# Optimization experiments

Hardware: AMD Instinct MI355X
Metric: run time of the kernel (lower is better)

## Reference

```python
import jax, jax.numpy as jnp
import numpy as np

THETA = 1.2
XI = 0.3


def setup_inputs() -> dict:
    key = jax.random.key(0)
    k1, k2 = jax.random.split(key)
    B, D = 8192, 512
    x = jax.random.normal(k1, (B, D), dtype=jnp.float32)
    y = jax.random.randint(k2, (B,), 0, 1000, dtype=jnp.int64)
    return {"x": x, "y": y}


def reference(x, y):
    B = x.shape[0]
    # per-sample L2 normalization: n_i = x_i / ||x_i||
    n = x / jnp.linalg.norm(x, axis=1, keepdims=True)  # [B, D]
    # pairwise squared distances ||n_i - n_j||^2 = |n_i|^2 + |n_j|^2 - 2 n_i.n_j
    sq = jnp.sum(n * n, axis=1)                        # [B]
    G = n @ n.T                                        # [B, B]
    dist2 = sq[:, None] + sq[None, :] - 2.0 * G        # [B, B]
    # indicator: +1 if same label else -1 (symmetric)
    ind = jnp.where(y[:, None] == y[None, :], 1.0, -1.0)
    # original loops i in [0,B), j in [i,B): upper triangle including diagonal
    idx = jnp.arange(B)
    mask = (idx[None, :] >= idx[:, None]).astype(x.dtype)
    hinge = jnp.maximum(THETA - dist2, 0.0)
    total = jnp.sum(mask * (XI + ind * hinge))
    m_scalar = 1.0 / (B * B - B)
    return m_scalar * total
```

## Files before the change

kernel.cpp:

```cpp
#include <hip/hip_runtime.h>
#include <cstdint>
#include <cstddef>

#define THETA 1.2f
#define XI 0.3f
#define BDIM 8192
#define DDIM 512
#define NWORK 544
#define NPAIRS_UP (((double)BDIM * (double)(BDIM + 1)) * 0.5)

typedef float f32x4 __attribute__((ext_vector_type(4)));
typedef int i32x8 __attribute__((ext_vector_type(8)));

__global__ __launch_bounds__(256) void normalize_rows(
    const float* __restrict__ x, unsigned char* __restrict__ nf8,
    float* __restrict__ sq, unsigned int* __restrict__ counter)
{
    if (blockIdx.x == 0 && threadIdx.x == 0) { *counter = 0u; }
    int row = blockIdx.x * 4 + (threadIdx.x >> 6);
    int l = threadIdx.x & 63;
    const float4* xr = (const float4*)(x + (size_t)row * DDIM);
    float4 f0 = xr[l];
    float4 f1 = xr[l + 64];
    float s = f0.x*f0.x + f0.y*f0.y + f0.z*f0.z + f0.w*f0.w
            + f1.x*f1.x + f1.y*f1.y + f1.z*f1.z + f1.w*f1.w;
    #pragma unroll
    for (int m = 1; m < 64; m <<= 1) s += __shfl_xor(s, m);
    float rn = rsqrtf(s);
    int pk0 = __builtin_amdgcn_cvt_pk_fp8_f32(f0.x * rn, f0.y * rn, 0, false);
    pk0     = __builtin_amdgcn_cvt_pk_fp8_f32(f0.z * rn, f0.w * rn, pk0, true);
    int pk1 = __builtin_amdgcn_cvt_pk_fp8_f32(f1.x * rn, f1.y * rn, 0, false);
    pk1     = __builtin_amdgcn_cvt_pk_fp8_f32(f1.z * rn, f1.w * rn, pk1, true);
    int* rowp = (int*)(nf8 + (size_t)row * DDIM);
    rowp[l] = pk0;
    rowp[l + 64] = pk1;
    if (l == 0) sq[row] = s * rn * rn;
}

__global__ __launch_bounds__(256) void gram_hinge(
    const unsigned char* __restrict__ nf8, const float* __restrict__ sq,
    const int* __restrict__ y, double* __restrict__ part,
    unsigned int* __restrict__ counter, float* __restrict__ out)
{
    int u = (NWORK - 1) - (int)blockIdx.x;
    int jg = (int)((sqrtf(1.0f + 2.0f * (float)u) - 1.0f) * 0.5f);
    while (2 * (jg + 1) * (jg + 2) <= u) ++jg;
    while (2 * jg * (jg + 1) > u) --jg;
    int bi = u - 2 * jg * (jg + 1);

    __shared__ unsigned char As[128 * 512];
    __shared__ float sqA[128];
    __shared__ int   yA[128];
    __shared__ float sqB[512];
    __shared__ int   yB[512];
    __shared__ float wpart[4];
    __shared__ double dpart[4];
    __shared__ int is_last;

    int tid = threadIdx.x;
    int w = tid >> 6, l = tid & 63;
    int wr = w >> 1, wc = w & 1;
    int lr = l & 15, q = l >> 4;

    const unsigned char* gA = nf8 + (size_t)bi * 128 * DDIM;
    {
        int rl = l >> 5;
        int gl = l & 31;
        #pragma unroll
        for (int i = 0; i < 16; ++i) {
            int rbase = w * 32 + i * 2;
            int r = rbase + rl;
            int gg = gl ^ (r & 7);
            __builtin_amdgcn_global_load_lds(
                (const __attribute__((address_space(1))) void*)(gA + (size_t)r * DDIM + gg * 16),
                (__attribute__((address_space(3))) void*)(As + rbase * 512), 16, 0, 0);
        }
    }
    {
        int arow = bi * 128;
        if (tid < 128) { sqA[tid] = sq[arow + tid]; yA[tid] = y[arow + tid]; }
        int cb = jg * 512;
        sqB[tid]       = sq[cb + tid];
        sqB[tid + 256] = sq[cb + tid + 256];
        yB[tid]        = y[cb + tid];
        yB[tid + 256]  = y[cb + tid + 256];
    }
    __syncthreads();

    float acc0 = 0.f, acc1 = 0.f, acc2 = 0.f, acc3 = 0.f;

    for (int jt = 0; jt < 4; ++jt) {
        int bj = jg * 4 + jt;
        if (bj < bi) continue;

        f32x4 accv[4][4] = {};
        const unsigned char* rowB =
            nf8 + ((size_t)(bj * 128 + wc * 64 + lr)) * DDIM + q * 32;

        i32x8 bfr[2][4];
        #pragma unroll
        for (int ni = 0; ni < 4; ++ni) {
            const int4* bp = (const int4*)(rowB + (size_t)ni * 16 * DDIM);
            int4 b0 = bp[0], b1 = bp[1];
            bfr[0][ni][0] = b0.x; bfr[0][ni][1] = b0.y; bfr[0][ni][2] = b0.z; bfr[0][ni][3] = b0.w;
            bfr[0][ni][4] = b1.x; bfr[0][ni][5] = b1.y; bfr[0][ni][6] = b1.z; bfr[0][ni][7] = b1.w;
        }

        #pragma unroll
        for (int it = 0; it < 4; ++it) {
            int cur = it & 1, nxt = cur ^ 1;
            if (it < 3) {
                int k1 = (it + 1) * 128;
                #pragma unroll
                for (int ni = 0; ni < 4; ++ni) {
                    const int4* bp = (const int4*)(rowB + (size_t)ni * 16 * DDIM + k1);
                    int4 b0 = bp[0], b1 = bp[1];
                    bfr[nxt][ni][0] = b0.x; bfr[nxt][ni][1] = b0.y;
                    bfr[nxt][ni][2] = b0.z; bfr[nxt][ni][3] = b0.w;
                    bfr[nxt][ni][4] = b1.x; bfr[nxt][ni][5] = b1.y;
                    bfr[nxt][ni][6] = b1.z; bfr[nxt][ni][7] = b1.w;
                }
            }
            i32x8 af[4];
            #pragma unroll
            for (int mi = 0; mi < 4; ++mi) {
                int r = wr * 64 + mi * 16 + lr;
                int G0 = it * 8 + q * 2;
                int sw = r & 7;
                int4 a0 = *(const int4*)(As + r * 512 + ((G0 ^ sw) << 4));
                int4 a1 = *(const int4*)(As + r * 512 + (((G0 | 1) ^ sw) << 4));
                af[mi][0] = a0.x; af[mi][1] = a0.y; af[mi][2] = a0.z; af[mi][3] = a0.w;
                af[mi][4] = a1.x; af[mi][5] = a1.y; af[mi][6] = a1.z; af[mi][7] = a1.w;
            }
            #pragma unroll
            for (int mi = 0; mi < 4; ++mi)
                #pragma unroll
                for (int ni = 0; ni < 4; ++ni)
                    accv[mi][ni] = __builtin_amdgcn_mfma_scale_f32_16x16x128_f8f6f4(
                        af[mi], bfr[cur][ni], accv[mi][ni],
                        0, 0, 0, 0x7F7F7F7F, 0, 0x7F7F7F7F);
        }

        int jrow = jt * 128 + wc * 64 + lr;
        float sqj[4]; int yj[4];
        #pragma unroll
        for (int ni = 0; ni < 4; ++ni) {
            sqj[ni] = sqB[jrow + ni * 16];
            yj[ni]  = yB[jrow + ni * 16];
        }
        if (bj != bi) {
            #pragma unroll
            for (int mi = 0; mi < 4; ++mi) {
                #pragma unroll
                for (int r = 0; r < 4; ++r) {
                    int ia = wr * 64 + mi * 16 + q * 4 + r;
                    float ci = THETA - sqA[ia];
                    int yi = yA[ia];
                    {
                        float h0 = fmaxf(fmaf(2.f, accv[mi][0][r], ci - sqj[0]), 0.f);
                        acc0 += (yi == yj[0]) ? h0 : -h0;
                        float h1 = fmaxf(fmaf(2.f, accv[mi][1][r], ci - sqj[1]), 0.f);
                        acc1 += (yi == yj[1]) ? h1 : -h1;
                        float h2 = fmaxf(fmaf(2.f, accv[mi][2][r], ci - sqj[2]), 0.f);
                        acc2 += (yi == yj[2]) ? h2 : -h2;
                        float h3 = fmaxf(fmaf(2.f, accv[mi][3][r], ci - sqj[3]), 0.f);
                        acc3 += (yi == yj[3]) ? h3 : -h3;
                    }
                }
            }
        } else {
            int cl0 = wc * 64 + lr;
            #pragma unroll
            for (int mi = 0; mi < 4; ++mi) {
                #pragma unroll
                for (int r = 0; r < 4; ++r) {
                    int rl_ = wr * 64 + mi * 16 + q * 4 + r;
                    int ia = rl_;
                    float ci = THETA - sqA[ia];
                    int yi = yA[ia];
                    #pragma unroll
                    for (int ni = 0; ni < 4; ++ni) {
                        float h = fmaxf(fmaf(2.f, accv[mi][ni][r], ci - sqj[ni]), 0.f);
                        float sh = (yi == yj[ni]) ? h : -h;
                        if (cl0 + ni * 16 >= rl_) acc0 += sh;
                    }
                }
            }
        }
    }

    float local = (acc0 + acc1) + (acc2 + acc3);
    #pragma unroll
    for (int off = 32; off > 0; off >>= 1) local += __shfl_down(local, off);
    if (l == 0) wpart[w] = local;
    __syncthreads();
    if (tid == 0) {
        double ssum = (double)wpart[0] + (double)wpart[1]
                    + (double)wpart[2] + (double)wpart[3];
        __hip_atomic_store(&part[blockIdx.x], ssum, __ATOMIC_RELEASE, __HIP_MEMORY_SCOPE_AGENT);
        unsigned int ticket = __hip_atomic_fetch_add(
            counter, 1u, __ATOMIC_ACQ_REL, __HIP_MEMORY_SCOPE_AGENT);
        is_last = (ticket == NWORK - 1) ? 1 : 0;
    }
    __syncthreads();
    if (is_last) {
        double s = 0.0;
        for (int i = tid; i < NWORK; i += 256)
            s += __hip_atomic_load(&part[i], __ATOMIC_ACQUIRE, __HIP_MEMORY_SCOPE_AGENT);
        #pragma unroll
        for (int off = 32; off > 0; off >>= 1) s += __shfl_down(s, off);
        if (l == 0) dpart[w] = s;
        __syncthreads();
        if (tid == 0) {
            double total = (dpart[0] + dpart[1] + dpart[2] + dpart[3])
                         + (double)XI * NPAIRS_UP;
            const double m = 1.0 / ((double)BDIM * (double)BDIM - (double)BDIM);
            out[0] = (float)(total * m);
        }
    }
}

extern "C" void kernel_launch(void* const* d_in, const int* in_sizes, int n_in,
                              void* d_out, int out_size, void* d_ws, size_t ws_size,
                              hipStream_t stream) {
    const float* x = (const float*)d_in[0];
    const int* y = (const int*)d_in[1];
    float* out = (float*)d_out;

    unsigned char* nf8 = (unsigned char*)d_ws;
    char* p = (char*)d_ws + (size_t)BDIM * DDIM;
    float* sq = (float*)p;
    unsigned int* counter = (unsigned int*)(p + (size_t)BDIM * 4);
    double* part = (double*)(p + (size_t)BDIM * 4 + 64);

    normalize_rows<<<BDIM / 4, 256, 0, stream>>>(x, nf8, sq, counter);
    gram_hinge<<<NWORK, 256, 0, stream>>>(nf8, sq, y, part, counter, out);
}
```

Before: 129.1 us.

## Use 512-thread blocks splitting column tiles across eight waves, drop B double-buffer

The gram_hinge kernel now launches 512 threads (8 waves) per block instead of 256. Each wave handles two 64x64 subtiles in two passes, so the four 128-column tiles are spread across more waves and the per-wave serial loop shrinks. The register double-buffering of B fragments is removed and B is loaded just before use, with A fragments read per mi. This lowers register pressure to fit the larger block and adds latency hiding through more waves, at the cost of losing explicit prefetch overlap.

Measured after the change: 132.8 us. 2.8% more time.

```diff
diff --git a/kernel.cpp b/kernel.cpp
--- a/kernel.cpp
+++ b/kernel.cpp
@@ -37,7 +37,7 @@
     if (l == 0) sq[row] = s * rn * rn;
 }
 
-__global__ __launch_bounds__(256) void gram_hinge(
+__global__ __launch_bounds__(512) void gram_hinge(
     const unsigned char* __restrict__ nf8, const float* __restrict__ sq,
     const int* __restrict__ y, double* __restrict__ part,
     unsigned int* __restrict__ counter, float* __restrict__ out)
@@ -53,13 +53,12 @@
     __shared__ int   yA[128];
     __shared__ float sqB[512];
     __shared__ int   yB[512];
-    __shared__ float wpart[4];
-    __shared__ double dpart[4];
+    __shared__ float wpart[8];
+    __shared__ double dpart[8];
     __shared__ int is_last;
 
     int tid = threadIdx.x;
     int w = tid >> 6, l = tid & 63;
-    int wr = w >> 1, wc = w & 1;
     int lr = l & 15, q = l >> 4;
 
     const unsigned char* gA = nf8 + (size_t)bi * 128 * DDIM;
@@ -67,8 +66,8 @@
         int rl = l >> 5;
         int gl = l & 31;
         #pragma unroll
-        for (int i = 0; i < 16; ++i) {
-            int rbase = w * 32 + i * 2;
+        for (int i = 0; i < 8; ++i) {
+            int rbase = w * 16 + i * 2;
             int r = rbase + rl;
             int gg = gl ^ (r & 7);
             __builtin_amdgcn_global_load_lds(
@@ -80,16 +79,19 @@
         int arow = bi * 128;
         if (tid < 128) { sqA[tid] = sq[arow + tid]; yA[tid] = y[arow + tid]; }
         int cb = jg * 512;
-        sqB[tid]       = sq[cb + tid];
-        sqB[tid + 256] = sq[cb + tid + 256];
-        yB[tid]        = y[cb + tid];
-        yB[tid + 256]  = y[cb + tid + 256];
+        sqB[tid] = sq[cb + tid];
+        yB[tid]  = y[cb + tid];
     }
     __syncthreads();
 
     float acc0 = 0.f, acc1 = 0.f, acc2 = 0.f, acc3 = 0.f;
 
-    for (int jt = 0; jt < 4; ++jt) {
+    #pragma unroll 1
+    for (int pass = 0; pass < 2; ++pass) {
+        int s = w + pass * 8;
+        int jt = s >> 2;
+        int quad = s & 3;
+        int wr = quad >> 1, wc = quad & 1;
         int bj = jg * 4 + jt;
         if (bj < bi) continue;
 
@@ -97,31 +99,17 @@
         const unsigned char* rowB =
             nf8 + ((size_t)(bj * 128 + wc * 64 + lr)) * DDIM + q * 32;
 
-        i32x8 bfr[2][4];
-        #pragma unroll
-        for (int ni = 0; ni < 4; ++ni) {
-            const int4* bp = (const int4*)(rowB + (size_t)ni * 16 * DDIM);
-            int4 b0 = bp[0], b1 = bp[1];
-            bfr[0][ni][0] = b0.x; bfr[0][ni][1] = b0.y; bfr[0][ni][2] = b0.z; bfr[0][ni][3] = b0.w;
-            bfr[0][ni][4] = b1.x; bfr[0][ni][5] = b1.y; bfr[0][ni][6] = b1.z; bfr[0][ni][7] = b1.w;
-        }
-
         #pragma unroll
         for (int it = 0; it < 4; ++it) {
-            int cur = it & 1, nxt = cur ^ 1;
-            if (it < 3) {
-                int k1 = (it + 1) * 128;
-                #pragma unroll
-                for (int ni = 0; ni < 4; ++ni) {
-                    const int4* bp = (const int4*)(rowB + (size_t)ni * 16 * DDIM + k1);
-                    int4 b0 = bp[0], b1 = bp[1];
-                    bfr[nxt][ni][0] = b0.x; bfr[nxt][ni][1] = b0.y;
-                    bfr[nxt][ni][2] = b0.z; bfr[nxt][ni][3] = b0.w;
-                    bfr[nxt][ni][4] = b1.x; bfr[nxt][ni][5] = b1.y;
-                    bfr[nxt][ni][6] = b1.z; bfr[nxt][ni][7] = b1.w;
-                }
-            }
-            i32x8 af[4];
+            int k0 = it * 128;
+            i32x8 bfr[4];
+            #pragma unroll
+            for (int ni = 0; ni < 4; ++ni) {
+                const int4* bp = (const int4*)(rowB + (size_t)ni * 16 * DDIM + k0);
+                int4 b0 = bp[0], b1 = bp[1];
+                bfr[ni][0] = b0.x; bfr[ni][1] = b0.y; bfr[ni][2] = b0.z; bfr[ni][3] = b0.w;
+                bfr[ni][4] = b1.x; bfr[ni][5] = b1.y; bfr[ni][6] = b1.z; bfr[ni][7] = b1.w;
+            }
             #pragma unroll
             for (int mi = 0; mi < 4; ++mi) {
                 int r = wr * 64 + mi * 16 + lr;
@@ -129,16 +117,15 @@
                 int sw = r & 7;
                 int4 a0 = *(const int4*)(As + r * 512 + ((G0 ^ sw) << 4));
                 int4 a1 = *(const int4*)(As + r * 512 + (((G0 | 1) ^ sw) << 4));
-                af[mi][0] = a0.x; af[mi][1] = a0.y; af[mi][2] = a0.z; af[mi][3] = a0.w;
-                af[mi][4] = a1.x; af[mi][5] = a1.y; af[mi][6] = a1.z; af[mi][7] = a1.w;
-            }
-            #pragma unroll
-            for (int mi = 0; mi < 4; ++mi)
+                i32x8 af;
+                af[0] = a0.x; af[1] = a0.y; af[2] = a0.z; af[3] = a0.w;
+                af[4] = a1.x; af[5] = a1.y; af[6] = a1.z; af[7] = a1.w;
                 #pragma unroll
                 for (int ni = 0; ni < 4; ++ni)
                     accv[mi][ni] = __builtin_amdgcn_mfma_scale_f32_16x16x128_f8f6f4(
-                        af[mi], bfr[cur][ni], accv[mi][ni],
+                        af, bfr[ni], accv[mi][ni],
                         0, 0, 0, 0x7F7F7F7F, 0, 0x7F7F7F7F);
+            }
         }
 
         int jrow = jt * 128 + wc * 64 + lr;
@@ -156,33 +143,30 @@
                     int ia = wr * 64 + mi * 16 + q * 4 + r;
                     float ci = THETA - sqA[ia];
                     int yi = yA[ia];
-                    {
-                        float h0 = fmaxf(fmaf(2.f, accv[mi][0][r], ci - sqj[0]), 0.f);
-                        acc0 += (yi == yj[0]) ? h0 : -h0;
-                        float h1 = fmaxf(fmaf(2.f, accv[mi][1][r], ci - sqj[1]), 0.f);
-                        acc1 += (yi == yj[1]) ? h1 : -h1;
-                        float h2 = fmaxf(fmaf(2.f, accv[mi][2][r], ci - sqj[2]), 0.f);
-                        acc2 += (yi == yj[2]) ? h2 : -h2;
-                        float h3 = fmaxf(fmaf(2.f, accv[mi][3][r], ci - sqj[3]), 0.f);
-                        acc3 += (yi == yj[3]) ? h3 : -h3;
-                    }
+                    float h0 = fmaxf(fmaf(2.f, accv[mi][0][r], ci - sqj[0]), 0.f);
+                    acc0 += (yi == yj[0]) ? h0 : -h0;
+                    float h1 = fmaxf(fmaf(2.f, accv[mi][1][r], ci - sqj[1]), 0.f);
+                    acc1 += (yi == yj[1]) ? h1 : -h1;
+                    float h2 = fmaxf(fmaf(2.f, accv[mi][2][r], ci - sqj[2]), 0.f);
+                    acc2 += (yi == yj[2]) ? h2 : -h2;
+                    float h3 = fmaxf(fmaf(2.f, accv[mi][3][r], ci - sqj[3]), 0.f);
+                    acc3 += (yi == yj[3]) ? h3 : -h3;
                 }
             }
         } else {
-            int cl0 = wc * 64 + lr;
             #pragma unroll
             for (int mi = 0; mi < 4; ++mi) {
                 #pragma unroll
                 for (int r = 0; r < 4; ++r) {
                     int rl_ = wr * 64 + mi * 16 + q * 4 + r;
-                    int ia = rl_;
-                    float ci = THETA - sqA[ia];
-                    int yi = yA[ia];
+                    float ci = THETA - sqA[rl_];
+                    int yi = yA[rl_];
                     #pragma unroll
                     for (int ni = 0; ni < 4; ++ni) {
+                        int cl = wc * 64 + lr + ni * 16;
                         float h = fmaxf(fmaf(2.f, accv[mi][ni][r], ci - sqj[ni]), 0.f);
                         float sh = (yi == yj[ni]) ? h : -h;
-                        if (cl0 + ni * 16 >= rl_) acc0 += sh;
+                        if (cl >= rl_) acc0 += sh;
                     }
                 }
             }
@@ -195,8 +179,9 @@
     if (l == 0) wpart[w] = local;
     __syncthreads();
     if (tid == 0) {
-        double ssum = (double)wpart[0] + (double)wpart[1]
-                    + (double)wpart[2] + (double)wpart[3];
+        double ssum = 0.0;
+        #pragma unroll
+        for (int i = 0; i < 8; ++i) ssum += (double)wpart[i];
         __hip_atomic_store(&part[blockIdx.x], ssum, __ATOMIC_RELEASE, __HIP_MEMORY_SCOPE_AGENT);
         unsigned int ticket = __hip_atomic_fetch_add(
             counter, 1u, __ATOMIC_ACQ_REL, __HIP_MEMORY_SCOPE_AGENT);
@@ -205,15 +190,17 @@
     __syncthreads();
     if (is_last) {
         double s = 0.0;
-        for (int i = tid; i < NWORK; i += 256)
+        for (int i = tid; i < NWORK; i += 512)
             s += __hip_atomic_load(&part[i], __ATOMIC_ACQUIRE, __HIP_MEMORY_SCOPE_AGENT);
         #pragma unroll
         for (int off = 32; off > 0; off >>= 1) s += __shfl_down(s, off);
         if (l == 0) dpart[w] = s;
         __syncthreads();
         if (tid == 0) {
-            double total = (dpart[0] + dpart[1] + dpart[2] + dpart[3])
-                         + (double)XI * NPAIRS_UP;
+            double total = 0.0;
+            #pragma unroll
+            for (int i = 0; i < 8; ++i) total += dpart[i];
+            total += (double)XI * NPAIRS_UP;
             const double m = 1.0 / ((double)BDIM * (double)BDIM - (double)BDIM);
             out[0] = (float)(total * m);
         }
@@ -234,5 +221,5 @@
     double* part = (double*)(p + (size_t)BDIM * 4 + 64);
 
     normalize_rows<<<BDIM / 4, 256, 0, stream>>>(x, nf8, sq, counter);
-    gram_hinge<<<NWORK, 256, 0, stream>>>(nf8, sq, y, part, counter, out);
+    gram_hinge<<<NWORK, 512, 0, stream>>>(nf8, sq, y, part, counter, out);
 }
```
